# Kernel optimization log

Hardware: AMD Instinct MI355X
Metric: run time of the kernel (lower is better)

Reference implementation:

```python
import jax, jax.numpy as jnp
import numpy as np

L, B, D = 512, 16, 256
H = 4            # MAX_DIFF == num_heads
MAX_BONDS = 6
MAX_DIFF = 4
PROB_SHIFT = 0.3


def _attn_weights(x, Wqk, Wq, bq, Wk, bk, mask):
    """Per-head softmax(QK^T/sqrt(hd)) with key padding mask.
    x: [b,l,d]; Wqk: [d,2d] (the inc/dec_qk pre-projection);
    Wq/Wk: [d,d] (MHA in_proj, stored x@W layout); mask: [b,l] bool (True=masked).
    Returns [b,h,l,l]. The V path / out_proj of the torch MHA are discarded
    by the original module, so they are omitted here.
    """
    b, l, d = x.shape
    hd = d // H
    q = x @ Wqk[:, :d]
    k = x @ Wqk[:, d:]
    Q = (q @ Wq + bq).reshape(b, l, H, hd)
    K = (k @ Wk + bk).reshape(b, l, H, hd)
    scores = jnp.einsum('blhd,bmhd->bhlm', Q, K) / np.sqrt(hd)
    scores = jnp.where(mask[:, None, None, :], -jnp.inf, scores)
    return jax.nn.softmax(scores, axis=-1)


def setup_inputs() -> dict:
    key = jax.random.key(0)
    ks = jax.random.split(key, 16)
    s = 0.05
    p = lambda k, shape: jax.random.normal(k, shape, jnp.float32) * s
    # key_padding_mask: last 64 positions padded (True == masked)
    src_mask = jnp.broadcast_to(jnp.arange(L)[None, :] >= (L - 64), (B, L))
    return {
        'molecule_embedding': jax.random.normal(ks[0], (L, B, D), jnp.float32),
        'src_bond': jax.random.randint(ks[1], (B, L, MAX_BONDS), 0, L, jnp.int32),
        'src_mask': src_mask,
        'W_inc_qk': p(ks[2], (D, 2 * D)),
        'Wq_inc': p(ks[3], (D, D)), 'bq_inc': p(ks[4], (D,)),
        'Wk_inc': p(ks[5], (D, D)), 'bk_inc': p(ks[6], (D,)),
        'W_dec_qk': p(ks[7], (D, 2 * D)),
        'Wq_dec': p(ks[8], (D, D)), 'bq_dec': p(ks[9], (D,)),
        'Wk_dec': p(ks[10], (D, D)), 'bk_dec': p(ks[11], (D,)),
        'Wc': p(ks[12], (MAX_DIFF, MAX_DIFF)), 'bc': p(ks[13], (MAX_DIFF,)),
    }


def reference(molecule_embedding, src_bond, src_mask,
              W_inc_qk, Wq_inc, bq_inc, Wk_inc, bk_inc,
              W_dec_qk, Wq_dec, bq_dec, Wk_dec, bk_dec,
              Wc, bc):
    x = jnp.transpose(molecule_embedding, (1, 0, 2))  # [b,l,d]
    b, l, _ = x.shape

    inc = _attn_weights(x, W_inc_qk, Wq_inc, bq_inc, Wk_inc, bk_inc, src_mask)
    dec = _attn_weights(x, W_dec_qk, Wq_dec, bq_dec, Wk_dec, bk_dec, src_mask)

    pad = (~src_mask).astype(jnp.float32)              # 1 - mask
    pm2 = pad[:, :, None] * pad[:, None, :]            # [b,l,l]

    # cls_layer((inc-dec).permute(0,2,3,1)) * (MAX_DIFF*pad_mask)[...,None]
    diff = (jnp.einsum('bhlm,hc->blmc', inc - dec, Wc) + bc)
    diff = diff * (MAX_DIFF * pm2)[..., None]          # [b,l,l,4]

    # src_bond has last dim == MAX_BONDS -> one-hot neighbor counts
    src_w = jax.nn.one_hot(src_bond, l, dtype=jnp.float32).sum(axis=2) * pm2  # [b,l,l]
    eye = jnp.eye(l, dtype=jnp.float32)
    src_w = src_w * (1.0 - eye)[None]                  # zero diagonal

    # _shift_probs(src_weight.long(), prob_shift, MAX_DIFF)
    oh = jax.nn.one_hot(src_w.astype(jnp.int32), MAX_DIFF, dtype=jnp.float32)
    probs = oh * (1.0 - PROB_SHIFT) + (1.0 - oh) * (PROB_SHIFT / (MAX_DIFF - 1))
    probs = probs / probs.sum(axis=-1, keepdims=True)

    return jnp.log(probs + 1e-6) + diff                # [b,l,l,4]
```

## Files before the change

kernel.cpp:

```cpp
#include <hip/hip_runtime.h>
#include <stdint.h>

typedef unsigned short u16t;
typedef short s8v __attribute__((ext_vector_type(8)));
typedef float f4v __attribute__((ext_vector_type(4)));

#define MFMA16 __builtin_amdgcn_mfma_f32_16x16x32_bf16

#define QKN (16*4*512*64)

__device__ __forceinline__ u16t f2bf(float f) {
  unsigned u = __builtin_bit_cast(unsigned, f);
  u += 0x7fffu + ((u >> 16) & 1u);
  return (u16t)(u >> 16);
}

__global__ __launch_bounds__(256) void mask_norm(const int* __restrict__ raw,
                                                 int* __restrict__ dst) {
  __shared__ int mode;
  const int t = threadIdx.x;
  if (t == 0) mode = 0;
  __syncthreads();
  unsigned v0 = (unsigned)raw[t], v1 = (unsigned)raw[t + 256];
  if (v0 == 0x3F800000u || v1 == 0x3F800000u) mode = 2;
  __syncthreads();
  if (mode == 0 && (v0 > 1u || v1 > 1u)) mode = 1;
  __syncthreads();
  const int i = blockIdx.x * 256 + t;
  int m;
  if (mode == 2)      m = (((const float*)raw)[i] != 0.0f) ? 1 : 0;
  else if (mode == 1) m = ((const unsigned char*)raw)[i];
  else                m = raw[i];
  dst[i] = m;
}

__global__ __launch_bounds__(256) void weff_kernel(
    const float* __restrict__ Wiqk, const float* __restrict__ Wqi, const float* __restrict__ Wki,
    const float* __restrict__ Wdqk, const float* __restrict__ Wqd, const float* __restrict__ Wkd,
    u16t* __restrict__ weffT) {
  __shared__ float At[16][65];
  __shared__ float Bt[16][65];
  const int tid = threadIdx.x;
  const int n0 = blockIdx.x * 64;
  const int d0 = blockIdx.y * 64;
  const int p  = blockIdx.z;
  const float* A2  = (p == 0) ? Wqi : (p == 1) ? Wki : (p == 2) ? Wqd : Wkd;
  const float* Wqk = (p < 2) ? Wiqk : Wdqk;
  const int aoff = (p & 1) * 256;
  const int tx = tid & 15, ty = tid >> 4;

  float acc[4][4];
#pragma unroll
  for (int i = 0; i < 4; ++i)
#pragma unroll
    for (int j = 0; j < 4; ++j) acc[i][j] = 0.f;

  for (int k0 = 0; k0 < 256; k0 += 16) {
    __syncthreads();
    {
      int nn = tid & 63, kr = tid >> 6;
#pragma unroll
      for (int pass = 0; pass < 4; ++pass) {
        int kk = kr + pass * 4;
        At[kk][nn] = A2[(size_t)(k0 + kk) * 256 + n0 + nn];
      }
      int kk = tid & 15, dr = tid >> 4;
#pragma unroll
      for (int pass = 0; pass < 4; ++pass) {
        int dd = dr + pass * 16;
        Bt[kk][dd] = Wqk[(size_t)(d0 + dd) * 512 + aoff + k0 + kk];
      }
    }
    __syncthreads();
#pragma unroll
    for (int kk = 0; kk < 16; ++kk) {
      float a[4], b[4];
#pragma unroll
      for (int i = 0; i < 4; ++i) a[i] = At[kk][ty * 4 + i];
#pragma unroll
      for (int j = 0; j < 4; ++j) b[j] = Bt[kk][tx * 4 + j];
#pragma unroll
      for (int i = 0; i < 4; ++i)
#pragma unroll
        for (int j = 0; j < 4; ++j) acc[i][j] = fmaf(a[i], b[j], acc[i][j]);
    }
  }

#pragma unroll
  for (int i = 0; i < 4; ++i) {
    u16t h[4] = {f2bf(acc[i][0]), f2bf(acc[i][1]), f2bf(acc[i][2]), f2bf(acc[i][3])};
    *(uint2*)(&weffT[((size_t)(p * 256 + n0 + ty * 4 + i)) * 256 + d0 + tx * 4]) =
        *(const uint2*)h;
  }
}

__global__ __launch_bounds__(256) void proj_kernel(
    const float* __restrict__ emb, const u16t* __restrict__ weffT,
    const float* __restrict__ bq_inc, const float* __restrict__ bk_inc,
    const float* __restrict__ bq_dec, const float* __restrict__ bk_dec,
    u16t* __restrict__ qk) {
  __shared__ __align__(16) u16t As[128 * 40];
  __shared__ __align__(16) u16t Bs[128 * 40];
  const int t = threadIdx.x;
  const int n0 = blockIdx.x * 128;
  const int r0 = blockIdx.y * 128;
  const int bb = r0 >> 9;
  const int l0 = r0 & 511;
  const int lane = t & 63, wid = t >> 6;
  const int quad = lane >> 4, c15 = lane & 15;
  const int wm = wid >> 1, wn = wid & 1;

  f4v acc[4][4];
#pragma unroll
  for (int i = 0; i < 4; ++i)
#pragma unroll
    for (int j = 0; j < 4; ++j) acc[i][j] = f4v{0.f, 0.f, 0.f, 0.f};

  for (int k0 = 0; k0 < 256; k0 += 32) {
    __syncthreads();
#pragma unroll
    for (int i = 0; i < 2; ++i) {
      int c = t + i * 256;
      int m = c >> 2, off = (c & 3) * 8;
      const float* src = emb + (size_t)((l0 + m) * 16 + bb) * 256 + k0 + off;
      float4 x0 = *(const float4*)src;
      float4 x1 = *(const float4*)(src + 4);
      u16t h[8] = {f2bf(x0.x), f2bf(x0.y), f2bf(x0.z), f2bf(x0.w),
                   f2bf(x1.x), f2bf(x1.y), f2bf(x1.z), f2bf(x1.w)};
      *(uint4*)(&As[m * 40 + off]) = *(const uint4*)h;
      *(uint4*)(&Bs[m * 40 + off]) =
          *(const uint4*)(weffT + (size_t)(n0 + m) * 256 + k0 + off);
    }
    __syncthreads();
    s8v af[4], bf[4];
#pragma unroll
    for (int mi = 0; mi < 4; ++mi)
      af[mi] = *(const s8v*)(&As[(wm * 64 + mi * 16 + c15) * 40 + quad * 8]);
#pragma unroll
    for (int ni = 0; ni < 4; ++ni)
      bf[ni] = *(const s8v*)(&Bs[(wn * 64 + ni * 16 + c15) * 40 + quad * 8]);
#pragma unroll
    for (int mi = 0; mi < 4; ++mi)
#pragma unroll
      for (int ni = 0; ni < 4; ++ni)
        acc[mi][ni] = MFMA16(af[mi], bf[ni], acc[mi][ni], 0, 0, 0);
  }

  const float* biasP[4] = {bq_inc, bk_inc, bq_dec, bk_dec};
#pragma unroll
  for (int ni = 0; ni < 4; ++ni) {
    int n = n0 + wn * 64 + ni * 16 + c15;
    int p = n >> 8, h = (n >> 6) & 3, tt = n & 63, jj = n & 255;
    float bias = biasP[p][jj];
    u16t* dst = qk + (size_t)p * QKN;
#pragma unroll
    for (int mi = 0; mi < 4; ++mi) {
#pragma unroll
      for (int reg = 0; reg < 4; ++reg) {
        int l = l0 + wm * 64 + mi * 16 + quad * 4 + reg;
        dst[((size_t)(bb * 4 + h) * 512 + l) * 64 + tt] = f2bf(acc[mi][ni][reg] + bias);
      }
    }
  }
}

__global__ __launch_bounds__(256) void stats_kernel(
    const u16t* __restrict__ qk, const int* __restrict__ mask, float* __restrict__ invsum) {
  __shared__ __align__(16) u16t Qs[64 * 72];
  __shared__ __align__(16) u16t Ks[128 * 72];
  __shared__ int mrow[512];
  const int t = threadIdx.x;
  const int l0 = blockIdx.x * 64;
  const int cy = blockIdx.y;
  const int pp = cy >> 6, bb = (cy >> 2) & 15, h = cy & 3;
  const u16t* Q = qk + (size_t)(2 * pp) * QKN;
  const u16t* K = qk + (size_t)(2 * pp + 1) * QKN;
  mrow[t] = mask[bb * 512 + t];
  mrow[t + 256] = mask[bb * 512 + t + 256];
#pragma unroll
  for (int i = 0; i < 2; ++i) {
    int c = t + i * 256;
    int row = c >> 3, off = (c & 7) * 8;
    *(uint4*)(&Qs[row * 72 + off]) =
        *(const uint4*)(Q + ((size_t)(bb * 4 + h) * 512 + l0 + row) * 64 + off);
  }
  const int lane = t & 63, wid = t >> 6;
  const int quad = lane >> 4, c15 = lane & 15;
  float rs[4] = {0.f, 0.f, 0.f, 0.f};
  for (int m0 = 0; m0 < 512; m0 += 128) {
    __syncthreads();
#pragma unroll
    for (int i = 0; i < 4; ++i) {
      int c = t + i * 256;
      int row = c >> 3, off = (c & 7) * 8;
      *(uint4*)(&Ks[row * 72 + off]) =
          *(const uint4*)(K + ((size_t)(bb * 4 + h) * 512 + m0 + row) * 64 + off);
    }
    __syncthreads();
    s8v a0 = *(const s8v*)(&Qs[(wid * 16 + c15) * 72 + quad * 8]);
    s8v a1 = *(const s8v*)(&Qs[(wid * 16 + c15) * 72 + 32 + quad * 8]);
#pragma unroll
    for (int nt = 0; nt < 8; ++nt) {
      s8v b0 = *(const s8v*)(&Ks[(nt * 16 + c15) * 72 + quad * 8]);
      s8v b1 = *(const s8v*)(&Ks[(nt * 16 + c15) * 72 + 32 + quad * 8]);
      f4v sacc = f4v{0.f, 0.f, 0.f, 0.f};
      sacc = MFMA16(a0, b0, sacc, 0, 0, 0);
      sacc = MFMA16(a1, b1, sacc, 0, 0, 0);
      int m = m0 + nt * 16 + c15;
      if (!mrow[m]) {
#pragma unroll
        for (int reg = 0; reg < 4; ++reg) rs[reg] += __expf(sacc[reg] * 0.125f);
      }
    }
  }
#pragma unroll
  for (int reg = 0; reg < 4; ++reg) {
#pragma unroll
    for (int off = 1; off < 16; off <<= 1) rs[reg] += __shfl_xor(rs[reg], off);
  }
  if (c15 == 0) {
#pragma unroll
    for (int reg = 0; reg < 4; ++reg) {
      int l = l0 + wid * 16 + quad * 4 + reg;
      invsum[((size_t)(pp * 16 + bb) * 4 + h) * 512 + l] = 1.0f / rs[reg];
    }
  }
}

__global__ __launch_bounds__(256) void final_kernel(
    const u16t* __restrict__ qk, const int* __restrict__ mask, const float* __restrict__ invsum,
    const int* __restrict__ src_bond, const float* __restrict__ Wc, const float* __restrict__ bc,
    float* __restrict__ out) {
  __shared__ __align__(16) u16t Qs[8 * 16 * 72];
  __shared__ __align__(16) u16t Ks[128 * 72];
  __shared__ int bondsL[96];
  __shared__ int mlds[144];
  const int t = threadIdx.x;
  const int m0 = blockIdx.x * 128;
  const int l0 = blockIdx.y * 16;
  const int bb = blockIdx.z;

#pragma unroll
  for (int i = 0; i < 4; ++i) {
    int c = t + i * 256;
    int q = c >> 7, row = (c >> 3) & 15, off = (c & 7) * 8;
    const u16t* Qb = qk + (size_t)(2 * (q >> 2)) * QKN;
    *(uint4*)(&Qs[(q * 16 + row) * 72 + off]) =
        *(const uint4*)(Qb + ((size_t)(bb * 4 + (q & 3)) * 512 + l0 + row) * 64 + off);
  }
  if (t < 96) bondsL[t] = src_bond[(size_t)(bb * 512 + l0 + t / 6) * 6 + (t % 6)];
  if (t < 128) mlds[t] = mask[bb * 512 + m0 + t];
  else if (t < 144) mlds[t] = mask[bb * 512 + l0 + (t - 128)];

  const int lane = t & 63, wid = t >> 6;
  const int quad = lane >> 4, c15 = lane & 15;

  float Wf[16];
#pragma unroll
  for (int i = 0; i < 16; ++i) Wf[i] = Wc[i];

  float dacc[2][4][4];
#pragma unroll
  for (int a = 0; a < 2; ++a)
#pragma unroll
    for (int r = 0; r < 4; ++r)
#pragma unroll
      for (int c = 0; c < 4; ++c) dacc[a][r][c] = 0.f;

  for (int q = 0; q < 8; ++q) {
    const int pp = q >> 2, h = q & 3;
    __syncthreads();
#pragma unroll
    for (int i = 0; i < 4; ++i) {
      int c = t + i * 256;
      int row = c >> 3, off = (c & 7) * 8;
      const u16t* Kb = qk + (size_t)(2 * pp + 1) * QKN;
      *(uint4*)(&Ks[row * 72 + off]) =
          *(const uint4*)(Kb + ((size_t)(bb * 4 + h) * 512 + m0 + row) * 64 + off);
    }
    __syncthreads();
    s8v a0 = *(const s8v*)(&Qs[(q * 16 + c15) * 72 + quad * 8]);
    s8v a1 = *(const s8v*)(&Qs[(q * 16 + c15) * 72 + 32 + quad * 8]);
    float iv[4];
#pragma unroll
    for (int reg = 0; reg < 4; ++reg)
      iv[reg] = invsum[((size_t)(pp * 16 + bb) * 4 + h) * 512 + l0 + quad * 4 + reg];
#pragma unroll
    for (int nt = 0; nt < 2; ++nt) {
      int nrow = wid * 32 + nt * 16 + c15;
      s8v b0 = *(const s8v*)(&Ks[nrow * 72 + quad * 8]);
      s8v b1 = *(const s8v*)(&Ks[nrow * 72 + 32 + quad * 8]);
      f4v sacc = f4v{0.f, 0.f, 0.f, 0.f};
      sacc = MFMA16(a0, b0, sacc, 0, 0, 0);
      sacc = MFMA16(a1, b1, sacc, 0, 0, 0);
      if (!mlds[nrow]) {
#pragma unroll
        for (int reg = 0; reg < 4; ++reg) {
          float P = __expf(sacc[reg] * 0.125f) * iv[reg];
          if (pp) P = -P;
#pragma unroll
          for (int c = 0; c < 4; ++c)
            dacc[nt][reg][c] = fmaf(P, Wf[h * 4 + c], dacc[nt][reg][c]);
        }
      }
    }
  }

  float bcF[4];
#pragma unroll
  for (int c = 0; c < 4; ++c) bcF[c] = bc[c];
  const float lgH = logf(0.7f + 1e-6f);
  const float lgM = logf(0.1f + 1e-6f);
  const float lgU = logf(0.25f + 1e-6f);

#pragma unroll
  for (int nt = 0; nt < 2; ++nt) {
    int mloc = wid * 32 + nt * 16 + c15;
    int m = m0 + mloc;
    bool padm = (mlds[mloc] == 0);
#pragma unroll
    for (int reg = 0; reg < 4; ++reg) {
      int lloc = quad * 4 + reg;
      int l = l0 + lloc;
      bool padl = (mlds[128 + lloc] == 0);
      bool pm = padl && padm;
      int cnt = 0;
#pragma unroll
      for (int j = 0; j < 6; ++j) cnt += (bondsL[lloc * 6 + j] == m) ? 1 : 0;
      int cls = (pm && (m != l)) ? cnt : 0;
      float v[4];
#pragma unroll
      for (int c = 0; c < 4; ++c) {
        float lp = (cls >= 4) ? lgU : ((c == cls) ? lgH : lgM);
        float dv = pm ? 4.f * (dacc[nt][reg][c] + bcF[c]) : 0.f;
        v[c] = lp + dv;
      }
      float4 o = make_float4(v[0], v[1], v[2], v[3]);
      *(float4*)(&out[((size_t)(bb * 512 + l) * 512 + m) * 4]) = o;
    }
  }
}

extern "C" void kernel_launch(void* const* d_in, const int* in_sizes, int n_in,
                              void* d_out, int out_size, void* d_ws, size_t ws_size,
                              hipStream_t stream) {
  (void)in_sizes; (void)n_in; (void)out_size; (void)ws_size;
  const float* emb      = (const float*)d_in[0];
  const int*   src_bond = (const int*)d_in[1];
  const int*   mask_raw = (const int*)d_in[2];
  const float* W_inc_qk = (const float*)d_in[3];
  const float* Wq_inc   = (const float*)d_in[4];
  const float* bq_inc   = (const float*)d_in[5];
  const float* Wk_inc   = (const float*)d_in[6];
  const float* bk_inc   = (const float*)d_in[7];
  const float* W_dec_qk = (const float*)d_in[8];
  const float* Wq_dec   = (const float*)d_in[9];
  const float* bq_dec   = (const float*)d_in[10];
  const float* Wk_dec   = (const float*)d_in[11];
  const float* bk_dec   = (const float*)d_in[12];
  const float* Wc       = (const float*)d_in[13];
  const float* bc       = (const float*)d_in[14];
  float* out = (float*)d_out;

  char* ws = (char*)d_ws;
  int*   wsMask = (int*)ws;
  u16t*  weffT  = (u16t*)(ws + 32768);
  u16t*  qk     = (u16t*)(ws + 32768 + 524288);
  float* invsum = (float*)(ws + 32768 + 524288 + 16777216);

  hipLaunchKernelGGL(mask_norm,   dim3(32),         dim3(256), 0, stream, mask_raw, wsMask);
  hipLaunchKernelGGL(weff_kernel, dim3(4, 4, 4),    dim3(256), 0, stream,
                     W_inc_qk, Wq_inc, Wk_inc, W_dec_qk, Wq_dec, Wk_dec, weffT);
  hipLaunchKernelGGL(proj_kernel, dim3(8, 64),      dim3(256), 0, stream,
                     emb, weffT, bq_inc, bk_inc, bq_dec, bk_dec, qk);
  hipLaunchKernelGGL(stats_kernel, dim3(8, 128),    dim3(256), 0, stream, qk, wsMask, invsum);
  hipLaunchKernelGGL(final_kernel, dim3(4, 32, 16), dim3(256), 0, stream,
                     qk, wsMask, invsum, src_bond, Wc, bc, out);
}
```

Measured before the change: 180.8 us.

## Enlarge query tiles in stats and final kernels to reuse K tiles

The stats kernel now handles 128 query rows per block instead of 64, so each wave computes two 16-row tiles against every loaded K tile. The final kernel handles 32 query rows per block instead of 16 and loads the Q tile and inverse sums per head inside the loop rather than preloading all eight heads. Both changes halve the grid and the number of times K is reloaded from global memory. In exchange each thread holds more accumulator registers and fewer blocks are launched, which may reduce occupancy.

```diff
diff --git a/kernel.cpp b/kernel.cpp
--- a/kernel.cpp
+++ b/kernel.cpp
@@ -166,64 +166,74 @@
 
 __global__ __launch_bounds__(256) void stats_kernel(
     const u16t* __restrict__ qk, const int* __restrict__ mask, float* __restrict__ invsum) {
-  __shared__ __align__(16) u16t Qs[64 * 72];
+  __shared__ __align__(16) u16t Qs[128 * 72];
   __shared__ __align__(16) u16t Ks[128 * 72];
   __shared__ int mrow[512];
   const int t = threadIdx.x;
-  const int l0 = blockIdx.x * 64;
+  const int l0 = blockIdx.x * 128;
   const int cy = blockIdx.y;
   const int pp = cy >> 6, bb = (cy >> 2) & 15, h = cy & 3;
-  const u16t* Q = qk + (size_t)(2 * pp) * QKN;
-  const u16t* K = qk + (size_t)(2 * pp + 1) * QKN;
+  const u16t* Q = qk + (size_t)(2 * pp) * QKN + ((size_t)(bb * 4 + h) * 512 + l0) * 64;
+  const u16t* K = qk + (size_t)(2 * pp + 1) * QKN + ((size_t)(bb * 4 + h) * 512) * 64;
   mrow[t] = mask[bb * 512 + t];
   mrow[t + 256] = mask[bb * 512 + t + 256];
 #pragma unroll
-  for (int i = 0; i < 2; ++i) {
+  for (int i = 0; i < 4; ++i) {
     int c = t + i * 256;
     int row = c >> 3, off = (c & 7) * 8;
-    *(uint4*)(&Qs[row * 72 + off]) =
-        *(const uint4*)(Q + ((size_t)(bb * 4 + h) * 512 + l0 + row) * 64 + off);
+    *(uint4*)(&Qs[row * 72 + off]) = *(const uint4*)(Q + row * 64 + off);
   }
   const int lane = t & 63, wid = t >> 6;
   const int quad = lane >> 4, c15 = lane & 15;
-  float rs[4] = {0.f, 0.f, 0.f, 0.f};
+  float rs[2][4] = {{0.f, 0.f, 0.f, 0.f}, {0.f, 0.f, 0.f, 0.f}};
   for (int m0 = 0; m0 < 512; m0 += 128) {
     __syncthreads();
 #pragma unroll
     for (int i = 0; i < 4; ++i) {
       int c = t + i * 256;
       int row = c >> 3, off = (c & 7) * 8;
-      *(uint4*)(&Ks[row * 72 + off]) =
-          *(const uint4*)(K + ((size_t)(bb * 4 + h) * 512 + m0 + row) * 64 + off);
-    }
-    __syncthreads();
-    s8v a0 = *(const s8v*)(&Qs[(wid * 16 + c15) * 72 + quad * 8]);
-    s8v a1 = *(const s8v*)(&Qs[(wid * 16 + c15) * 72 + 32 + quad * 8]);
+      *(uint4*)(&Ks[row * 72 + off]) = *(const uint4*)(K + (size_t)(m0 + row) * 64 + off);
+    }
+    __syncthreads();
+    s8v a[2][2];
+#pragma unroll
+    for (int lt = 0; lt < 2; ++lt) {
+      a[lt][0] = *(const s8v*)(&Qs[(wid * 32 + lt * 16 + c15) * 72 + quad * 8]);
+      a[lt][1] = *(const s8v*)(&Qs[(wid * 32 + lt * 16 + c15) * 72 + 32 + quad * 8]);
+    }
 #pragma unroll
     for (int nt = 0; nt < 8; ++nt) {
       s8v b0 = *(const s8v*)(&Ks[(nt * 16 + c15) * 72 + quad * 8]);
       s8v b1 = *(const s8v*)(&Ks[(nt * 16 + c15) * 72 + 32 + quad * 8]);
-      f4v sacc = f4v{0.f, 0.f, 0.f, 0.f};
-      sacc = MFMA16(a0, b0, sacc, 0, 0, 0);
-      sacc = MFMA16(a1, b1, sacc, 0, 0, 0);
       int m = m0 + nt * 16 + c15;
-      if (!mrow[m]) {
-#pragma unroll
-        for (int reg = 0; reg < 4; ++reg) rs[reg] += __expf(sacc[reg] * 0.125f);
-      }
-    }
-  }
-#pragma unroll
-  for (int reg = 0; reg < 4; ++reg) {
-#pragma unroll
-    for (int off = 1; off < 16; off <<= 1) rs[reg] += __shfl_xor(rs[reg], off);
-  }
+      bool valid = !mrow[m];
+#pragma unroll
+      for (int lt = 0; lt < 2; ++lt) {
+        f4v sacc = f4v{0.f, 0.f, 0.f, 0.f};
+        sacc = MFMA16(a[lt][0], b0, sacc, 0, 0, 0);
+        sacc = MFMA16(a[lt][1], b1, sacc, 0, 0, 0);
+        if (valid) {
+#pragma unroll
+          for (int reg = 0; reg < 4; ++reg) rs[lt][reg] += __expf(sacc[reg] * 0.125f);
+        }
+      }
+    }
+  }
+#pragma unroll
+  for (int lt = 0; lt < 2; ++lt)
+#pragma unroll
+    for (int reg = 0; reg < 4; ++reg) {
+#pragma unroll
+      for (int off = 1; off < 16; off <<= 1) rs[lt][reg] += __shfl_xor(rs[lt][reg], off);
+    }
   if (c15 == 0) {
 #pragma unroll
-    for (int reg = 0; reg < 4; ++reg) {
-      int l = l0 + wid * 16 + quad * 4 + reg;
-      invsum[((size_t)(pp * 16 + bb) * 4 + h) * 512 + l] = 1.0f / rs[reg];
-    }
+    for (int lt = 0; lt < 2; ++lt)
+#pragma unroll
+      for (int reg = 0; reg < 4; ++reg) {
+        int l = l0 + wid * 32 + lt * 16 + quad * 4 + reg;
+        invsum[((size_t)(pp * 16 + bb) * 4 + h) * 512 + l] = 1.0f / rs[lt][reg];
+      }
   }
 }
 
@@ -231,26 +241,19 @@
     const u16t* __restrict__ qk, const int* __restrict__ mask, const float* __restrict__ invsum,
     const int* __restrict__ src_bond, const float* __restrict__ Wc, const float* __restrict__ bc,
     float* __restrict__ out) {
-  __shared__ __align__(16) u16t Qs[8 * 16 * 72];
+  __shared__ __align__(16) u16t Qs[32 * 72];
   __shared__ __align__(16) u16t Ks[128 * 72];
-  __shared__ int bondsL[96];
-  __shared__ int mlds[144];
+  __shared__ float ivs[32];
+  __shared__ int bondsL[192];
+  __shared__ int mlds[160];
   const int t = threadIdx.x;
   const int m0 = blockIdx.x * 128;
-  const int l0 = blockIdx.y * 16;
+  const int l0 = blockIdx.y * 32;
   const int bb = blockIdx.z;
 
-#pragma unroll
-  for (int i = 0; i < 4; ++i) {
-    int c = t + i * 256;
-    int q = c >> 7, row = (c >> 3) & 15, off = (c & 7) * 8;
-    const u16t* Qb = qk + (size_t)(2 * (q >> 2)) * QKN;
-    *(uint4*)(&Qs[(q * 16 + row) * 72 + off]) =
-        *(const uint4*)(Qb + ((size_t)(bb * 4 + (q & 3)) * 512 + l0 + row) * 64 + off);
-  }
-  if (t < 96) bondsL[t] = src_bond[(size_t)(bb * 512 + l0 + t / 6) * 6 + (t % 6)];
+  if (t < 192) bondsL[t] = src_bond[(size_t)(bb * 512 + l0 + t / 6) * 6 + (t % 6)];
   if (t < 128) mlds[t] = mask[bb * 512 + m0 + t];
-  else if (t < 144) mlds[t] = mask[bb * 512 + l0 + (t - 128)];
+  else if (t < 160) mlds[t] = mask[bb * 512 + l0 + (t - 128)];
 
   const int lane = t & 63, wid = t >> 6;
   const int quad = lane >> 4, c15 = lane & 15;
@@ -259,48 +262,66 @@
 #pragma unroll
   for (int i = 0; i < 16; ++i) Wf[i] = Wc[i];
 
-  float dacc[2][4][4];
+  float dacc[2][2][4][4];
 #pragma unroll
   for (int a = 0; a < 2; ++a)
 #pragma unroll
-    for (int r = 0; r < 4; ++r)
-#pragma unroll
-      for (int c = 0; c < 4; ++c) dacc[a][r][c] = 0.f;
+    for (int b2 = 0; b2 < 2; ++b2)
+#pragma unroll
+      for (int r = 0; r < 4; ++r)
+#pragma unroll
+        for (int c = 0; c < 4; ++c) dacc[a][b2][r][c] = 0.f;
 
   for (int q = 0; q < 8; ++q) {
     const int pp = q >> 2, h = q & 3;
     __syncthreads();
+    const u16t* Kb = qk + (size_t)(2 * pp + 1) * QKN + ((size_t)(bb * 4 + h) * 512 + m0) * 64;
 #pragma unroll
     for (int i = 0; i < 4; ++i) {
       int c = t + i * 256;
       int row = c >> 3, off = (c & 7) * 8;
-      const u16t* Kb = qk + (size_t)(2 * pp + 1) * QKN;
-      *(uint4*)(&Ks[row * 72 + off]) =
-          *(const uint4*)(Kb + ((size_t)(bb * 4 + h) * 512 + m0 + row) * 64 + off);
-    }
-    __syncthreads();
-    s8v a0 = *(const s8v*)(&Qs[(q * 16 + c15) * 72 + quad * 8]);
-    s8v a1 = *(const s8v*)(&Qs[(q * 16 + c15) * 72 + 32 + quad * 8]);
-    float iv[4];
-#pragma unroll
-    for (int reg = 0; reg < 4; ++reg)
-      iv[reg] = invsum[((size_t)(pp * 16 + bb) * 4 + h) * 512 + l0 + quad * 4 + reg];
-#pragma unroll
-    for (int nt = 0; nt < 2; ++nt) {
-      int nrow = wid * 32 + nt * 16 + c15;
-      s8v b0 = *(const s8v*)(&Ks[nrow * 72 + quad * 8]);
-      s8v b1 = *(const s8v*)(&Ks[nrow * 72 + 32 + quad * 8]);
-      f4v sacc = f4v{0.f, 0.f, 0.f, 0.f};
-      sacc = MFMA16(a0, b0, sacc, 0, 0, 0);
-      sacc = MFMA16(a1, b1, sacc, 0, 0, 0);
-      if (!mlds[nrow]) {
-#pragma unroll
-        for (int reg = 0; reg < 4; ++reg) {
-          float P = __expf(sacc[reg] * 0.125f) * iv[reg];
-          if (pp) P = -P;
-#pragma unroll
-          for (int c = 0; c < 4; ++c)
-            dacc[nt][reg][c] = fmaf(P, Wf[h * 4 + c], dacc[nt][reg][c]);
+      *(uint4*)(&Ks[row * 72 + off]) = *(const uint4*)(Kb + row * 64 + off);
+    }
+    {
+      const u16t* Qb = qk + (size_t)(2 * pp) * QKN + ((size_t)(bb * 4 + h) * 512 + l0) * 64;
+      int row = t >> 3, off = (t & 7) * 8;
+      *(uint4*)(&Qs[row * 72 + off]) = *(const uint4*)(Qb + row * 64 + off);
+    }
+    if (t < 32) ivs[t] = invsum[((size_t)(pp * 16 + bb) * 4 + h) * 512 + l0 + t];
+    __syncthreads();
+
+    s8v a[2][2];
+#pragma unroll
+    for (int lt = 0; lt < 2; ++lt) {
+      a[lt][0] = *(const s8v*)(&Qs[(lt * 16 + c15) * 72 + quad * 8]);
+      a[lt][1] = *(const s8v*)(&Qs[(lt * 16 + c15) * 72 + 32 + quad * 8]);
+    }
+    float iv[2][4];
+#pragma unroll
+    for (int lt = 0; lt < 2; ++lt)
+#pragma unroll
+      for (int reg = 0; reg < 4; ++reg) iv[lt][reg] = ivs[lt * 16 + quad * 4 + reg];
+
+#pragma unroll
+    for (int mt = 0; mt < 2; ++mt) {
+      int mloc = wid * 32 + mt * 16 + c15;
+      s8v b0 = *(const s8v*)(&Ks[mloc * 72 + quad * 8]);
+      s8v b1 = *(const s8v*)(&Ks[mloc * 72 + 32 + quad * 8]);
+      bool valid = !mlds[mloc];
+#pragma unroll
+      for (int lt = 0; lt < 2; ++lt) {
+        f4v sacc = f4v{0.f, 0.f, 0.f, 0.f};
+        sacc = MFMA16(a[lt][0], b0, sacc, 0, 0, 0);
+        sacc = MFMA16(a[lt][1], b1, sacc, 0, 0, 0);
+        if (valid) {
+#pragma unroll
+          for (int reg = 0; reg < 4; ++reg) {
+            float P = __expf(sacc[reg] * 0.125f) * iv[lt][reg];
+            if (pp) P = -P;
+#pragma unroll
+            for (int c = 0; c < 4; ++c)
+              dacc[lt][mt][reg][c] = fmaf(P, Wf[h * 4 + c], dacc[lt][mt][reg][c]);
+          }
         }
       }
     }
@@ -314,29 +335,32 @@
   const float lgU = logf(0.25f + 1e-6f);
 
 #pragma unroll
-  for (int nt = 0; nt < 2; ++nt) {
-    int mloc = wid * 32 + nt * 16 + c15;
+  for (int mt = 0; mt < 2; ++mt) {
+    int mloc = wid * 32 + mt * 16 + c15;
     int m = m0 + mloc;
     bool padm = (mlds[mloc] == 0);
 #pragma unroll
-    for (int reg = 0; reg < 4; ++reg) {
-      int lloc = quad * 4 + reg;
-      int l = l0 + lloc;
-      bool padl = (mlds[128 + lloc] == 0);
-      bool pm = padl && padm;
-      int cnt = 0;
-#pragma unroll
-      for (int j = 0; j < 6; ++j) cnt += (bondsL[lloc * 6 + j] == m) ? 1 : 0;
-      int cls = (pm && (m != l)) ? cnt : 0;
-      float v[4];
-#pragma unroll
-      for (int c = 0; c < 4; ++c) {
-        float lp = (cls >= 4) ? lgU : ((c == cls) ? lgH : lgM);
-        float dv = pm ? 4.f * (dacc[nt][reg][c] + bcF[c]) : 0.f;
-        v[c] = lp + dv;
-      }
-      float4 o = make_float4(v[0], v[1], v[2], v[3]);
-      *(float4*)(&out[((size_t)(bb * 512 + l) * 512 + m) * 4]) = o;
+    for (int lt = 0; lt < 2; ++lt) {
+#pragma unroll
+      for (int reg = 0; reg < 4; ++reg) {
+        int lloc = lt * 16 + quad * 4 + reg;
+        int l = l0 + lloc;
+        bool padl = (mlds[128 + lloc] == 0);
+        bool pm = padl && padm;
+        int cnt = 0;
+#pragma unroll
+        for (int j = 0; j < 6; ++j) cnt += (bondsL[lloc * 6 + j] == m) ? 1 : 0;
+        int cls = (pm && (m != l)) ? cnt : 0;
+        float v[4];
+#pragma unroll
+        for (int c = 0; c < 4; ++c) {
+          float lp = (cls >= 4) ? lgU : ((c == cls) ? lgH : lgM);
+          float dv = pm ? 4.f * (dacc[lt][mt][reg][c] + bcF[c]) : 0.f;
+          v[c] = lp + dv;
+        }
+        float4 o = make_float4(v[0], v[1], v[2], v[3]);
+        *(float4*)(&out[((size_t)(bb * 512 + l) * 512 + m) * 4]) = o;
+      }
     }
   }
 }
@@ -373,7 +397,7 @@
                      W_inc_qk, Wq_inc, Wk_inc, W_dec_qk, Wq_dec, Wk_dec, weffT);
   hipLaunchKernelGGL(proj_kernel, dim3(8, 64),      dim3(256), 0, stream,
                      emb, weffT, bq_inc, bk_inc, bq_dec, bk_dec, qk);
-  hipLaunchKernelGGL(stats_kernel, dim3(8, 128),    dim3(256), 0, stream, qk, wsMask, invsum);
-  hipLaunchKernelGGL(final_kernel, dim3(4, 32, 16), dim3(256), 0, stream,
+  hipLaunchKernelGGL(stats_kernel, dim3(4, 128),    dim3(256), 0, stream, qk, wsMask, invsum);
+  hipLaunchKernelGGL(final_kernel, dim3(4, 16, 16), dim3(256), 0, stream,
                      qk, wsMask, invsum, src_bond, Wc, bc, out);
 }
```

Measured after the change: 192.3 us. 1.06x slower.

## Drop LDS staging in stats and final kernels, load MFMA operands from global

Applied to the files above, without the earlier changes.

Both the stats and final kernels stop staging Q/K tiles in shared memory and instead load MFMA fragments straight from global memory, which removes the per-iteration __syncthreads barriers. The stats kernel is remapped so each wave owns a 32-row tile with its own key loop, and the launch becomes 512 blocks. Masking changes from a branch to multiplication by a 0/±1 factor. The cost is more uncoalesced 16-byte global/L2 reads and repeated K reads across waves, in exchange for no LDS traffic and no block-wide synchronisation.

```diff
diff --git a/kernel.cpp b/kernel.cpp
--- a/kernel.cpp
+++ b/kernel.cpp
@@ -166,64 +166,56 @@
 
 __global__ __launch_bounds__(256) void stats_kernel(
     const u16t* __restrict__ qk, const int* __restrict__ mask, float* __restrict__ invsum) {
-  __shared__ __align__(16) u16t Qs[64 * 72];
-  __shared__ __align__(16) u16t Ks[128 * 72];
-  __shared__ int mrow[512];
   const int t = threadIdx.x;
-  const int l0 = blockIdx.x * 64;
-  const int cy = blockIdx.y;
-  const int pp = cy >> 6, bb = (cy >> 2) & 15, h = cy & 3;
-  const u16t* Q = qk + (size_t)(2 * pp) * QKN;
-  const u16t* K = qk + (size_t)(2 * pp + 1) * QKN;
-  mrow[t] = mask[bb * 512 + t];
-  mrow[t + 256] = mask[bb * 512 + t + 256];
-#pragma unroll
-  for (int i = 0; i < 2; ++i) {
-    int c = t + i * 256;
-    int row = c >> 3, off = (c & 7) * 8;
-    *(uint4*)(&Qs[row * 72 + off]) =
-        *(const uint4*)(Q + ((size_t)(bb * 4 + h) * 512 + l0 + row) * 64 + off);
-  }
   const int lane = t & 63, wid = t >> 6;
   const int quad = lane >> 4, c15 = lane & 15;
-  float rs[4] = {0.f, 0.f, 0.f, 0.f};
-  for (int m0 = 0; m0 < 512; m0 += 128) {
-    __syncthreads();
-#pragma unroll
-    for (int i = 0; i < 4; ++i) {
-      int c = t + i * 256;
-      int row = c >> 3, off = (c & 7) * 8;
-      *(uint4*)(&Ks[row * 72 + off]) =
-          *(const uint4*)(K + ((size_t)(bb * 4 + h) * 512 + m0 + row) * 64 + off);
-    }
-    __syncthreads();
-    s8v a0 = *(const s8v*)(&Qs[(wid * 16 + c15) * 72 + quad * 8]);
-    s8v a1 = *(const s8v*)(&Qs[(wid * 16 + c15) * 72 + 32 + quad * 8]);
-#pragma unroll
-    for (int nt = 0; nt < 8; ++nt) {
-      s8v b0 = *(const s8v*)(&Ks[(nt * 16 + c15) * 72 + quad * 8]);
-      s8v b1 = *(const s8v*)(&Ks[(nt * 16 + c15) * 72 + 32 + quad * 8]);
+  const int w = blockIdx.x * 4 + wid;
+  const int lt = w & 15, cy = w >> 4;
+  const int pp = cy >> 6, bb = (cy >> 2) & 15, h = cy & 3;
+  const int l0 = lt * 32;
+
+  const u16t* Q = qk + (size_t)(2 * pp) * QKN + ((size_t)(bb * 4 + h) * 512 + l0) * 64;
+  const u16t* K = qk + (size_t)(2 * pp + 1) * QKN + ((size_t)(bb * 4 + h) * 512) * 64;
+  const int* mrow = mask + bb * 512;
+
+  s8v a[2][2];
+#pragma unroll
+  for (int j = 0; j < 2; ++j) {
+    a[j][0] = *(const s8v*)(Q + (j * 16 + c15) * 64 + quad * 8);
+    a[j][1] = *(const s8v*)(Q + (j * 16 + c15) * 64 + 32 + quad * 8);
+  }
+
+  float rs[2][4] = {{0.f, 0.f, 0.f, 0.f}, {0.f, 0.f, 0.f, 0.f}};
+  for (int m0 = 0; m0 < 512; m0 += 16) {
+    const u16t* Kr = K + (size_t)(m0 + c15) * 64 + quad * 8;
+    s8v b0 = *(const s8v*)(Kr);
+    s8v b1 = *(const s8v*)(Kr + 32);
+    float vm = mrow[m0 + c15] ? 0.f : 1.f;
+#pragma unroll
+    for (int j = 0; j < 2; ++j) {
       f4v sacc = f4v{0.f, 0.f, 0.f, 0.f};
-      sacc = MFMA16(a0, b0, sacc, 0, 0, 0);
-      sacc = MFMA16(a1, b1, sacc, 0, 0, 0);
-      int m = m0 + nt * 16 + c15;
-      if (!mrow[m]) {
-#pragma unroll
-        for (int reg = 0; reg < 4; ++reg) rs[reg] += __expf(sacc[reg] * 0.125f);
-      }
-    }
-  }
-#pragma unroll
-  for (int reg = 0; reg < 4; ++reg) {
-#pragma unroll
-    for (int off = 1; off < 16; off <<= 1) rs[reg] += __shfl_xor(rs[reg], off);
-  }
+      sacc = MFMA16(a[j][0], b0, sacc, 0, 0, 0);
+      sacc = MFMA16(a[j][1], b1, sacc, 0, 0, 0);
+#pragma unroll
+      for (int reg = 0; reg < 4; ++reg)
+        rs[j][reg] += vm * __expf(sacc[reg] * 0.125f);
+    }
+  }
+#pragma unroll
+  for (int j = 0; j < 2; ++j)
+#pragma unroll
+    for (int reg = 0; reg < 4; ++reg) {
+#pragma unroll
+      for (int off = 1; off < 16; off <<= 1) rs[j][reg] += __shfl_xor(rs[j][reg], off);
+    }
   if (c15 == 0) {
 #pragma unroll
-    for (int reg = 0; reg < 4; ++reg) {
-      int l = l0 + wid * 16 + quad * 4 + reg;
-      invsum[((size_t)(pp * 16 + bb) * 4 + h) * 512 + l] = 1.0f / rs[reg];
-    }
+    for (int j = 0; j < 2; ++j)
+#pragma unroll
+      for (int reg = 0; reg < 4; ++reg) {
+        int l = l0 + j * 16 + quad * 4 + reg;
+        invsum[((size_t)(pp * 16 + bb) * 4 + h) * 512 + l] = 1.0f / rs[j][reg];
+      }
   }
 }
 
@@ -231,29 +223,24 @@
     const u16t* __restrict__ qk, const int* __restrict__ mask, const float* __restrict__ invsum,
     const int* __restrict__ src_bond, const float* __restrict__ Wc, const float* __restrict__ bc,
     float* __restrict__ out) {
-  __shared__ __align__(16) u16t Qs[8 * 16 * 72];
-  __shared__ __align__(16) u16t Ks[128 * 72];
   __shared__ int bondsL[96];
-  __shared__ int mlds[144];
+  __shared__ int padls[16];
   const int t = threadIdx.x;
   const int m0 = blockIdx.x * 128;
   const int l0 = blockIdx.y * 16;
   const int bb = blockIdx.z;
 
-#pragma unroll
-  for (int i = 0; i < 4; ++i) {
-    int c = t + i * 256;
-    int q = c >> 7, row = (c >> 3) & 15, off = (c & 7) * 8;
-    const u16t* Qb = qk + (size_t)(2 * (q >> 2)) * QKN;
-    *(uint4*)(&Qs[(q * 16 + row) * 72 + off]) =
-        *(const uint4*)(Qb + ((size_t)(bb * 4 + (q & 3)) * 512 + l0 + row) * 64 + off);
-  }
   if (t < 96) bondsL[t] = src_bond[(size_t)(bb * 512 + l0 + t / 6) * 6 + (t % 6)];
-  if (t < 128) mlds[t] = mask[bb * 512 + m0 + t];
-  else if (t < 144) mlds[t] = mask[bb * 512 + l0 + (t - 128)];
+  else if (t < 112) padls[t - 96] = mask[bb * 512 + l0 + (t - 96)];
+  __syncthreads();
 
   const int lane = t & 63, wid = t >> 6;
   const int quad = lane >> 4, c15 = lane & 15;
+  const int mw = m0 + wid * 32;
+
+  int mval[2];
+  mval[0] = mask[bb * 512 + mw + c15];
+  mval[1] = mask[bb * 512 + mw + 16 + c15];
 
   float Wf[16];
 #pragma unroll
@@ -269,39 +256,30 @@
 
   for (int q = 0; q < 8; ++q) {
     const int pp = q >> 2, h = q & 3;
-    __syncthreads();
-#pragma unroll
-    for (int i = 0; i < 4; ++i) {
-      int c = t + i * 256;
-      int row = c >> 3, off = (c & 7) * 8;
-      const u16t* Kb = qk + (size_t)(2 * pp + 1) * QKN;
-      *(uint4*)(&Ks[row * 72 + off]) =
-          *(const uint4*)(Kb + ((size_t)(bb * 4 + h) * 512 + m0 + row) * 64 + off);
-    }
-    __syncthreads();
-    s8v a0 = *(const s8v*)(&Qs[(q * 16 + c15) * 72 + quad * 8]);
-    s8v a1 = *(const s8v*)(&Qs[(q * 16 + c15) * 72 + 32 + quad * 8]);
+    const u16t* Qb = qk + (size_t)(2 * pp) * QKN + ((size_t)(bb * 4 + h) * 512 + l0) * 64;
+    const u16t* Kb = qk + (size_t)(2 * pp + 1) * QKN + ((size_t)(bb * 4 + h) * 512 + mw) * 64;
+    s8v a0 = *(const s8v*)(Qb + c15 * 64 + quad * 8);
+    s8v a1 = *(const s8v*)(Qb + c15 * 64 + 32 + quad * 8);
     float iv[4];
-#pragma unroll
-    for (int reg = 0; reg < 4; ++reg)
-      iv[reg] = invsum[((size_t)(pp * 16 + bb) * 4 + h) * 512 + l0 + quad * 4 + reg];
-#pragma unroll
-    for (int nt = 0; nt < 2; ++nt) {
-      int nrow = wid * 32 + nt * 16 + c15;
-      s8v b0 = *(const s8v*)(&Ks[nrow * 72 + quad * 8]);
-      s8v b1 = *(const s8v*)(&Ks[nrow * 72 + 32 + quad * 8]);
+    const float* ivb = invsum + ((size_t)(pp * 16 + bb) * 4 + h) * 512 + l0 + quad * 4;
+#pragma unroll
+    for (int reg = 0; reg < 4; ++reg) iv[reg] = ivb[reg];
+    const float sgn = pp ? -1.f : 1.f;
+#pragma unroll
+    for (int ms = 0; ms < 2; ++ms) {
+      const u16t* Kr = Kb + (ms * 16 + c15) * 64 + quad * 8;
+      s8v b0 = *(const s8v*)(Kr);
+      s8v b1 = *(const s8v*)(Kr + 32);
       f4v sacc = f4v{0.f, 0.f, 0.f, 0.f};
       sacc = MFMA16(a0, b0, sacc, 0, 0, 0);
       sacc = MFMA16(a1, b1, sacc, 0, 0, 0);
-      if (!mlds[nrow]) {
-#pragma unroll
-        for (int reg = 0; reg < 4; ++reg) {
-          float P = __expf(sacc[reg] * 0.125f) * iv[reg];
-          if (pp) P = -P;
-#pragma unroll
-          for (int c = 0; c < 4; ++c)
-            dacc[nt][reg][c] = fmaf(P, Wf[h * 4 + c], dacc[nt][reg][c]);
-        }
+      const float vm = mval[ms] ? 0.f : sgn;
+#pragma unroll
+      for (int reg = 0; reg < 4; ++reg) {
+        float P = __expf(sacc[reg] * 0.125f) * iv[reg] * vm;
+#pragma unroll
+        for (int c = 0; c < 4; ++c)
+          dacc[ms][reg][c] = fmaf(P, Wf[h * 4 + c], dacc[ms][reg][c]);
       }
     }
   }
@@ -314,16 +292,14 @@
   const float lgU = logf(0.25f + 1e-6f);
 
 #pragma unroll
-  for (int nt = 0; nt < 2; ++nt) {
-    int mloc = wid * 32 + nt * 16 + c15;
-    int m = m0 + mloc;
-    bool padm = (mlds[mloc] == 0);
+  for (int ms = 0; ms < 2; ++ms) {
+    int m = mw + ms * 16 + c15;
+    bool padm = (mval[ms] == 0);
 #pragma unroll
     for (int reg = 0; reg < 4; ++reg) {
       int lloc = quad * 4 + reg;
       int l = l0 + lloc;
-      bool padl = (mlds[128 + lloc] == 0);
-      bool pm = padl && padm;
+      bool pm = padm && (padls[lloc] == 0);
       int cnt = 0;
 #pragma unroll
       for (int j = 0; j < 6; ++j) cnt += (bondsL[lloc * 6 + j] == m) ? 1 : 0;
@@ -332,7 +308,7 @@
 #pragma unroll
       for (int c = 0; c < 4; ++c) {
         float lp = (cls >= 4) ? lgU : ((c == cls) ? lgH : lgM);
-        float dv = pm ? 4.f * (dacc[nt][reg][c] + bcF[c]) : 0.f;
+        float dv = pm ? 4.f * (dacc[ms][reg][c] + bcF[c]) : 0.f;
         v[c] = lp + dv;
       }
       float4 o = make_float4(v[0], v[1], v[2], v[3]);
@@ -373,7 +349,7 @@
                      W_inc_qk, Wq_inc, Wk_inc, W_dec_qk, Wq_dec, Wk_dec, weffT);
   hipLaunchKernelGGL(proj_kernel, dim3(8, 64),      dim3(256), 0, stream,
                      emb, weffT, bq_inc, bk_inc, bq_dec, bk_dec, qk);
-  hipLaunchKernelGGL(stats_kernel, dim3(8, 128),    dim3(256), 0, stream, qk, wsMask, invsum);
+  hipLaunchKernelGGL(stats_kernel, dim3(512),       dim3(256), 0, stream, qk, wsMask, invsum);
   hipLaunchKernelGGL(final_kernel, dim3(4, 32, 16), dim3(256), 0, stream,
                      qk, wsMask, invsum, src_bond, Wc, bc, out);
 }
```

Result: slower. 207.9 us (+15.0%).
